# Performance work log

Measured on AMD Instinct MI355X. Metric: run time of the kernel, lower is better.

Reference implementation:

```python
import jax, jax.numpy as jnp
import numpy as np

B, S, D, H = 2, 2048, 1024, 16
DK = D // H
ROPE_BASE = 10000.0


def _rope_cos_sin(seq_len, dim, dtype):
    inv_freq = 1.0 / (ROPE_BASE ** (jnp.arange(0, dim, 2, dtype=jnp.float32) / dim))
    t = jnp.arange(seq_len, dtype=jnp.float32)
    freqs = jnp.outer(t, inv_freq)              # [S, dim/2]
    emb = jnp.concatenate([freqs, freqs], -1)   # [S, dim]
    return jnp.cos(emb).astype(dtype), jnp.sin(emb).astype(dtype)


def _rotate_half(x):
    x1, x2 = jnp.split(x, 2, axis=-1)
    return jnp.concatenate([-x2, x1], axis=-1)


def setup_inputs() -> dict:
    key = jax.random.key(0)
    ks = jax.random.split(key, 7)
    q = jax.random.normal(ks[0], (B, S, D), jnp.float32)
    k = jax.random.normal(ks[1], (B, S, D), jnp.float32)
    v = jax.random.normal(ks[2], (B, S, D), jnp.float32)
    scale = 0.02
    Wq = jax.random.normal(ks[3], (D, D), jnp.float32) * scale
    Wk = jax.random.normal(ks[4], (D, D), jnp.float32) * scale
    Wv = jax.random.normal(ks[5], (D, D), jnp.float32) * scale
    Wo = jax.random.normal(ks[6], (D, D), jnp.float32) * scale
    mask = jnp.tril(jnp.ones((S, S), jnp.int32))[None, None]  # [1,1,S,S] causal 0/1
    return {"q": q, "k": k, "v": v, "Wq": Wq, "Wk": Wk, "Wv": Wv, "Wo": Wo, "mask": mask}


def reference(q, k, v, Wq, Wk, Wv, Wo, mask):
    def proj(x, W):
        # nn.Linear: x @ W.T ; then [B,S,H,DK] -> [B,H,S,DK]
        return (x @ W.T).reshape(B, S, H, DK).transpose(0, 2, 1, 3)

    qh, kh, vh = proj(q, Wq), proj(k, Wk), proj(v, Wv)

    cos, sin = _rope_cos_sin(S, DK, qh.dtype)   # [S, DK]
    qh = qh * cos + _rotate_half(qh) * sin
    kh = kh * cos + _rotate_half(kh) * sin

    scores = jnp.einsum("bhqd,bhkd->bhqk", qh, kh) / jnp.sqrt(jnp.asarray(DK, qh.dtype))
    scores = jnp.where(mask == 0, jnp.asarray(-1000.0, scores.dtype), scores)
    attn = jax.nn.softmax(scores, axis=-1)      # dropout=0 (eval)
    out = jnp.einsum("bhqk,bhkd->bhqd", attn, vh)
    out = out.transpose(0, 2, 1, 3).reshape(B, S, D)
    return out @ Wo.T
```

## Files before the change

### kernel.cpp

```cpp
#include <hip/hip_runtime.h>
#include <hip/hip_bf16.h>
#include <stdint.h>

#define Bdim 2
#define Sdim 2048
#define Ddim 1024
#define Hdim 16

typedef unsigned short u16;
typedef __bf16 bf16x8 __attribute__((ext_vector_type(8)));
typedef float f32x4 __attribute__((ext_vector_type(4)));

__device__ __forceinline__ u16 f2b(float x) {
  return __builtin_bit_cast(u16, (__bf16)x);
}
__device__ __forceinline__ float b2f(u16 u) {
  return __bfloat162float(__builtin_bit_cast(__hip_bfloat16, u));
}
__device__ __forceinline__ f32x4 mfma_bf16(bf16x8 a, bf16x8 b, f32x4 c) {
  return __builtin_amdgcn_mfma_f32_16x16x32_bf16(a, b, c, 0, 0, 0);
}
__device__ __forceinline__ void gload_lds16(const u16* gp, u16* lp) {
  __builtin_amdgcn_global_load_lds(
      (const __attribute__((address_space(1))) void*)gp,
      (__attribute__((address_space(3))) void*)lp, 16, 0, 0);
}

__global__ __launch_bounds__(256) void k_convert(
    const float* __restrict__ q, const float* __restrict__ k, const float* __restrict__ v,
    const float* __restrict__ wq, const float* __restrict__ wk,
    const float* __restrict__ wv, const float* __restrict__ wo,
    u16* __restrict__ qb, u16* __restrict__ kb, u16* __restrict__ vb,
    u16* __restrict__ wqb, u16* __restrict__ wkb, u16* __restrict__ wvb, u16* __restrict__ wob) {
  int i = (blockIdx.x * 256 + threadIdx.x) * 4;
  const float* src;
  u16* dst;
  int off;
  if (i < 12582912) {
    int s = i >> 22;
    off = i - (s << 22);
    src = (s == 0) ? q : ((s == 1) ? k : v);
    dst = (s == 0) ? qb : ((s == 1) ? kb : vb);
  } else {
    int j = i - 12582912;
    int s = j >> 20;
    off = j - (s << 20);
    src = (s == 0) ? wq : ((s == 1) ? wk : ((s == 2) ? wv : wo));
    dst = (s == 0) ? wqb : ((s == 1) ? wkb : ((s == 2) ? wvb : wob));
  }
  float4 f = *(const float4*)(src + off);
  ushort4 o;
  o.x = f2b(f.x); o.y = f2b(f.y); o.z = f2b(f.z); o.w = f2b(f.w);
  *(ushort4*)(dst + off) = o;
}

__global__ __launch_bounds__(256) void k_ropetab(float* __restrict__ cosT, float* __restrict__ sinT) {
  int i = blockIdx.x * 256 + threadIdx.x;
  int s = i >> 5, j = i & 31;
  float invf = expf(-(float)j * 0.28782313662425574f);
  float ang = (float)s * invf;
  float sn, cs;
  sincosf(ang, &sn, &cs);
  cosT[i] = cs;
  sinT[i] = sn;
}

template <int OUTF>
__global__ __launch_bounds__(256) void k_gemm(
    const u16* __restrict__ A0, const u16* __restrict__ W0, void* __restrict__ O0,
    const u16* __restrict__ A1, const u16* __restrict__ W1, void* __restrict__ O1,
    const u16* __restrict__ A2, const u16* __restrict__ W2, void* __restrict__ O2) {
  const u16* A = (blockIdx.z == 0) ? A0 : ((blockIdx.z == 1) ? A1 : A2);
  const u16* W = (blockIdx.z == 0) ? W0 : ((blockIdx.z == 1) ? W1 : W2);
  void* O = (blockIdx.z == 0) ? O0 : ((blockIdx.z == 1) ? O1 : O2);

  __shared__ u16 As[128 * 32];
  __shared__ u16 Bs[128 * 32];

  const int tid = threadIdx.x;
  const int wave = tid >> 6, lane = tid & 63;
  const int g = lane >> 4, cc = lane & 15;
  const int wm = wave >> 1, wn = wave & 1;
  const int row0 = blockIdx.x * 128, col0 = blockIdx.y * 128;

  const int srow = wave * 16 + (lane >> 2);
  const int sseg = (lane & 3) * 8;
  const u16* Ap  = A + (size_t)(row0 + srow) * 1024 + sseg;
  const u16* Ap2 = Ap + 64 * 1024;
  const u16* Wp  = W + (size_t)(col0 + srow) * 1024 + sseg;
  const u16* Wp2 = Wp + 64 * 1024;
  u16* asl  = &As[wave * 512];
  u16* asl2 = &As[2048 + wave * 512];
  u16* bsl  = &Bs[wave * 512];
  u16* bsl2 = &Bs[2048 + wave * 512];

  f32x4 acc[4][4] = {};

  for (int k0 = 0; k0 < 1024; k0 += 32) {
    __syncthreads();
    gload_lds16(Ap + k0, asl);
    gload_lds16(Ap2 + k0, asl2);
    gload_lds16(Wp + k0, bsl);
    gload_lds16(Wp2 + k0, bsl2);
    __syncthreads();
    bf16x8 af[4], bfv[4];
#pragma unroll
    for (int mi = 0; mi < 4; ++mi)
      af[mi] = *(const bf16x8*)&As[(wm * 64 + mi * 16 + cc) * 32 + g * 8];
#pragma unroll
    for (int ni = 0; ni < 4; ++ni)
      bfv[ni] = *(const bf16x8*)&Bs[(wn * 64 + ni * 16 + cc) * 32 + g * 8];
#pragma unroll
    for (int mi = 0; mi < 4; ++mi)
#pragma unroll
      for (int ni = 0; ni < 4; ++ni)
        acc[mi][ni] = mfma_bf16(af[mi], bfv[ni], acc[mi][ni]);
  }

#pragma unroll
  for (int mi = 0; mi < 4; ++mi)
#pragma unroll
    for (int ni = 0; ni < 4; ++ni)
#pragma unroll
      for (int r = 0; r < 4; ++r) {
        const int row = row0 + wm * 64 + mi * 16 + g * 4 + r;
        const int col = col0 + wn * 64 + ni * 16 + cc;
        const float vv = acc[mi][ni][r];
        if (OUTF)
          ((float*)O)[row * 1024 + col] = vv;
        else
          ((u16*)O)[row * 1024 + col] = f2b(vv);
      }
}

__global__ __launch_bounds__(256) void k_rope(
    const u16* __restrict__ tq, const u16* __restrict__ tk,
    const float* __restrict__ cosT, const float* __restrict__ sinT,
    u16* __restrict__ Qr, u16* __restrict__ Kr) {
  int idx = blockIdx.x * 256 + threadIdx.x;
  int t = idx >> 21;
  int r = idx & ((1 << 21) - 1);
  int j = r & 31;
  int h = (r >> 5) & 15;
  int s = (r >> 9) & 2047;
  int b = (r >> 20) & 1;

  const u16* in = t ? tk : tq;
  u16* out = t ? Kr : Qr;

  int bi = (b * Sdim + s) * Ddim + h * 64 + j;
  float x1 = b2f(in[bi]);
  float x2 = b2f(in[bi + 32]);
  float cv = cosT[s * 32 + j];
  float sv = sinT[s * 32 + j];
  float o1 = x1 * cv - x2 * sv;
  float o2 = x2 * cv + x1 * sv;
  if (t == 0) { o1 *= 0.18033688011112042f; o2 *= 0.18033688011112042f; }
  int bo = ((b * Hdim + h) * Sdim + s) * 64 + j;
  out[bo] = f2b(o1);
  out[bo + 32] = f2b(o2);
}

__global__ __launch_bounds__(256) void k_transv(const u16* __restrict__ tv, u16* __restrict__ Vt) {
  __shared__ u16 tl[64][72];
  const int bh = blockIdx.y;
  const int b = bh >> 4, h = bh & 15;
  const int s0 = blockIdx.x * 64;
  const int tid = threadIdx.x;
#pragma unroll
  for (int p = 0; p < 4; ++p) {
    int row = p * 16 + (tid >> 4);
    int dc = (tid & 15) * 4;
    ushort4 val = *(const ushort4*)(tv + (b * Sdim + s0 + row) * Ddim + h * 64 + dc);
    *(ushort4*)&tl[row][dc] = val;
  }
  __syncthreads();
#pragma unroll
  for (int p = 0; p < 4; ++p) {
    int dr = p * 16 + (tid >> 4);
    int sc = (tid & 15) * 4;
    ushort4 o;
    o.x = tl[sc + 0][dr];
    o.y = tl[sc + 1][dr];
    o.z = tl[sc + 2][dr];
    o.w = tl[sc + 3][dr];
    int s_abs = s0 + sc;
    int cch = s_abs >> 5;
    int kap = s_abs & 31;
    int g2 = (kap >> 2) & 3;
    int seg = kap >> 4;
    *(ushort4*)(Vt + (size_t)(bh * 64 + dr) * Sdim + (cch << 5) + (g2 << 3) + (seg << 2)) = o;
  }
}

template <int M0, int M1>
__device__ __forceinline__ void attn_chunk64(
    const u16* __restrict__ kl, const u16* __restrict__ vl, int cc, int g,
    const bf16x8 qf[4],
    float& mold0, float& mold1, float& lsum0, float& lsum1,
    f32x4 ot0[4], f32x4 ot1[4]) {
  const int m7 = cc & 7;
  const int gA = (g ^ m7) * 8;
  const int gB = ((g + 4) ^ m7) * 8;

  f32x4 x0A0 = {}, x0B0 = {}, x0A1 = {}, x0B1 = {};
  {
    const u16* r0 = kl + cc * 64;
    const u16* r1 = kl + (16 + cc) * 64;
    bf16x8 k0 = *(const bf16x8*)(r0 + gA);
    bf16x8 k1 = *(const bf16x8*)(r0 + gB);
    bf16x8 k2 = *(const bf16x8*)(r1 + gA);
    bf16x8 k3 = *(const bf16x8*)(r1 + gB);
    x0A0 = mfma_bf16(k0, qf[0], x0A0);
    x0A0 = mfma_bf16(k1, qf[1], x0A0);
    x0B0 = mfma_bf16(k2, qf[0], x0B0);
    x0B0 = mfma_bf16(k3, qf[1], x0B0);
    x0A1 = mfma_bf16(k0, qf[2], x0A1);
    x0A1 = mfma_bf16(k1, qf[3], x0A1);
    x0B1 = mfma_bf16(k2, qf[2], x0B1);
    x0B1 = mfma_bf16(k3, qf[3], x0B1);
  }
  f32x4 x1A0 = {}, x1B0 = {}, x1A1 = {}, x1B1 = {};
  if (M1 != 2) {
    const u16* r0 = kl + (32 + cc) * 64;
    const u16* r1 = kl + (48 + cc) * 64;
    bf16x8 k0 = *(const bf16x8*)(r0 + gA);
    bf16x8 k1 = *(const bf16x8*)(r0 + gB);
    bf16x8 k2 = *(const bf16x8*)(r1 + gA);
    bf16x8 k3 = *(const bf16x8*)(r1 + gB);
    x1A0 = mfma_bf16(k0, qf[0], x1A0);
    x1A0 = mfma_bf16(k1, qf[1], x1A0);
    x1B0 = mfma_bf16(k2, qf[0], x1B0);
    x1B0 = mfma_bf16(k3, qf[1], x1B0);
    x1A1 = mfma_bf16(k0, qf[2], x1A1);
    x1A1 = mfma_bf16(k1, qf[3], x1A1);
    x1B1 = mfma_bf16(k2, qf[2], x1B1);
    x1B1 = mfma_bf16(k3, qf[3], x1B1);
  }

  float p0[16], p1[16];
#pragma unroll
  for (int r = 0; r < 4; ++r) {
    const int ka = g * 4 + r;
    float a0 = x0A0[r], b0 = x0B0[r], a1 = x0A1[r], b1 = x0B1[r];
    if (M0 == 1) {
      a0 = (ka <= cc) ? a0 : -30000.0f;
      b0 = -30000.0f;
      b1 = (ka <= cc) ? b1 : -30000.0f;
    }
    p0[r] = a0; p0[4 + r] = b0;
    p1[r] = a1; p1[4 + r] = b1;
  }
  if (M1 != 2) {
#pragma unroll
    for (int r = 0; r < 4; ++r) {
      const int ka = g * 4 + r;
      float a0 = x1A0[r], b0 = x1B0[r], a1 = x1A1[r], b1 = x1B1[r];
      if (M1 == 1) {
        a0 = (ka <= cc) ? a0 : -30000.0f;
        b0 = -30000.0f;
        b1 = (ka <= cc) ? b1 : -30000.0f;
      }
      p0[8 + r] = a0; p0[12 + r] = b0;
      p1[8 + r] = a1; p1[12 + r] = b1;
    }
  }
  const int NP = (M1 == 2) ? 8 : 16;
  float m0 = p0[0], m1 = p1[0];
#pragma unroll
  for (int j = 1; j < 16; ++j)
    if (j < NP) { m0 = fmaxf(m0, p0[j]); m1 = fmaxf(m1, p1[j]); }

  if (!__all((m0 <= mold0 + 11.5f) && (m1 <= mold1 + 11.5f))) {
    float M0v = fmaxf(m0, __shfl_xor(m0, 16));
    M0v = fmaxf(M0v, __shfl_xor(M0v, 32));
    float M1v = fmaxf(m1, __shfl_xor(m1, 16));
    M1v = fmaxf(M1v, __shfl_xor(M1v, 32));
    M0v = fmaxf(mold0, M0v);
    M1v = fmaxf(mold1, M1v);
    const float al0 = exp2f(mold0 - M0v), al1 = exp2f(mold1 - M1v);
    mold0 = M0v; mold1 = M1v;
    lsum0 *= al0; lsum1 *= al1;
#pragma unroll
    for (int dc = 0; dc < 4; ++dc) { ot0[dc] *= al0; ot1[dc] *= al1; }
  }

  float rs0 = 0.f, rs1 = 0.f;
  bf16x8 a0v, a1v, b0v2, b1v2;
#pragma unroll
  for (int j = 0; j < 8; ++j) {
    float e0 = exp2f(p0[j] - mold0);
    float e1 = exp2f(p1[j] - mold1);
    rs0 += e0; rs1 += e1;
    a0v[j] = (__bf16)e0;
    a1v[j] = (__bf16)e1;
  }
  if (M1 != 2) {
#pragma unroll
    for (int j = 0; j < 8; ++j) {
      float e0 = exp2f(p0[8 + j] - mold0);
      float e1 = exp2f(p1[8 + j] - mold1);
      rs0 += e0; rs1 += e1;
      b0v2[j] = (__bf16)e0;
      b1v2[j] = (__bf16)e1;
    }
  }
  lsum0 += rs0; lsum1 += rs1;

#pragma unroll
  for (int dc = 0; dc < 4; ++dc) {
    bf16x8 vv = *(const bf16x8*)(vl + (dc * 16 + cc) * 64 + gA);
    ot0[dc] = mfma_bf16(vv, a0v, ot0[dc]);
    ot1[dc] = mfma_bf16(vv, a1v, ot1[dc]);
  }
  if (M1 != 2) {
#pragma unroll
    for (int dc = 0; dc < 4; ++dc) {
      bf16x8 vv = *(const bf16x8*)(vl + (dc * 16 + cc) * 64 + gB);
      ot0[dc] = mfma_bf16(vv, b0v2, ot0[dc]);
      ot1[dc] = mfma_bf16(vv, b1v2, ot1[dc]);
    }
  }
}

__global__ __launch_bounds__(256, 2) void k_attn(
    const u16* __restrict__ Qr, const u16* __restrict__ Kr,
    const u16* __restrict__ Vt, u16* __restrict__ Oc,
    float* __restrict__ PO, float* __restrict__ PML) {
  __shared__ u16 Kl[2][4096];
  __shared__ u16 Vl[2][4096];

  const int x = blockIdx.x;
  const int bh = x & 31;
  const int slot = x >> 5;
  const int p = slot & 7;
  const int half = slot >> 3;
  const int iH = 15 - p, iL = p;
  const int nH = 2 * iH + 2;
  const int b = bh >> 4, h = bh & 15;
  const int tid = threadIdx.x;
  const int w = tid >> 6;
  const int lane = tid & 63;
  const int g = lane >> 4, cc = lane & 15;

  const u16* Kp = Kr + (size_t)bh * (Sdim * 64);
  const u16* Vp = Vt + (size_t)bh * (64 * Sdim);

  const int rloc = lane >> 3;
  const int sg = (lane & 7) ^ rloc;
  const u16* kS = Kp + (size_t)(w * 16 + rloc) * 64 + sg * 8;
  const u16* vS = Vp + (size_t)(w * 16 + rloc) * 2048 + sg * 8;

  auto stageKV = [&](int t, int buf) {
    const size_t ko = (size_t)t * 4096;
    const size_t vo = (size_t)t * 64;
    gload_lds16(kS + ko, &Kl[buf][w * 1024]);
    gload_lds16(kS + ko + 512, &Kl[buf][w * 1024 + 512]);
    gload_lds16(vS + vo, &Vl[buf][w * 1024]);
    gload_lds16(vS + vo + 16384, &Vl[buf][w * 1024 + 512]);
  };

  auto runseg = [&](int tile, int c0, int c1, int part) {
    const int myDiag = 2 * tile + (w >> 1);
    const u16* Qp = Qr + (size_t)(bh * Sdim + tile * 128 + w * 32) * 64;
    bf16x8 qf[4];
    qf[0] = *(const bf16x8*)(Qp + cc * 64 + g * 8);
    qf[1] = *(const bf16x8*)(Qp + cc * 64 + g * 8 + 32);
    qf[2] = *(const bf16x8*)(Qp + (16 + cc) * 64 + g * 8);
    qf[3] = *(const bf16x8*)(Qp + (16 + cc) * 64 + g * 8 + 32);

    float mold0 = -1e30f, mold1 = -1e30f, lsum0 = 0.f, lsum1 = 0.f;
    f32x4 ot0[4] = {}, ot1[4] = {};

    __syncthreads();
    stageKV(c0, c0 & 1);
    for (int t = c0; t < c1; ++t) {
      __syncthreads();
      if (t + 1 < c1) stageKV(t + 1, (t + 1) & 1);
      if (t <= myDiag) {
        const u16* kl = &Kl[t & 1][0];
        const u16* vl = &Vl[t & 1][0];
        if (t < myDiag)
          attn_chunk64<0, 0>(kl, vl, cc, g, qf, mold0, mold1, lsum0, lsum1, ot0, ot1);
        else if (w & 1)
          attn_chunk64<0, 1>(kl, vl, cc, g, qf, mold0, mold1, lsum0, lsum1, ot0, ot1);
        else
          attn_chunk64<1, 2>(kl, vl, cc, g, qf, mold0, mold1, lsum0, lsum1, ot0, ot1);
      }
    }

    float l0 = lsum0 + __shfl_xor(lsum0, 16);
    l0 += __shfl_xor(l0, 32);
    float l1 = lsum1 + __shfl_xor(lsum1, 16);
    l1 += __shfl_xor(l1, 32);

    if (part < 0) {
      const float rl0 = 1.0f / l0, rl1 = 1.0f / l1;
      u16* dst0 = Oc + (size_t)(b * Sdim + tile * 128 + w * 32 + cc) * Ddim + h * 64 + g * 4;
      u16* dst1 = dst0 + 16 * Ddim;
#pragma unroll
      for (int dc = 0; dc < 4; ++dc) {
        ushort4 o0, o1;
        o0.x = f2b(ot0[dc][0] * rl0);
        o0.y = f2b(ot0[dc][1] * rl0);
        o0.z = f2b(ot0[dc][2] * rl0);
        o0.w = f2b(ot0[dc][3] * rl0);
        o1.x = f2b(ot1[dc][0] * rl1);
        o1.y = f2b(ot1[dc][1] * rl1);
        o1.z = f2b(ot1[dc][2] * rl1);
        o1.w = f2b(ot1[dc][3] * rl1);
        *(ushort4*)(dst0 + dc * 16) = o0;
        *(ushort4*)(dst1 + dc * 16) = o1;
      }
    } else {
      const int slotp = (bh * 7 + p) * 2 + part;
      float* po0 = PO + (size_t)slotp * 8192 + (w * 32 + cc) * 64;
      float* po1 = po0 + 16 * 64;
#pragma unroll
      for (int dc = 0; dc < 4; ++dc) {
        *(f32x4*)(po0 + dc * 16 + g * 4) = ot0[dc];
        *(f32x4*)(po1 + dc * 16 + g * 4) = ot1[dc];
      }
      if (g == 0) {
        float* ml = PML + (size_t)slotp * 256 + (w * 32 + cc) * 2;
        ml[0] = mold0;
        ml[1] = l0;
        ml[32] = mold1;
        ml[33] = l1;
      }
    }
  };

  if (half == 0) {
    runseg(iH, 0, (nH < 18) ? nH : 18, (nH > 18) ? 0 : -1);
  } else {
    if (p < 7) runseg(iH, 18, nH, 1);
    runseg(iL, 0, 2 * iL + 2, -1);
  }
}

__global__ __launch_bounds__(128) void k_comb(
    const float* __restrict__ PO, const float* __restrict__ PML,
    u16* __restrict__ Oc) {
  const int x = blockIdx.x;
  const int bh = x / 7, p = x % 7;
  const int b = bh >> 4, h = bh & 15;
  const int iH = 15 - p;
  const int row = threadIdx.x;
  const float* ml0 = PML + (size_t)(x * 2 + 0) * 256 + row * 2;
  const float* ml1 = PML + (size_t)(x * 2 + 1) * 256 + row * 2;
  const float m0 = ml0[0], l0 = ml0[1];
  const float m1 = ml1[0], l1 = ml1[1];
  const float M = fmaxf(m0, m1);
  float e0 = exp2f(m0 - M), e1 = exp2f(m1 - M);
  const float inv = 1.0f / (e0 * l0 + e1 * l1);
  e0 *= inv; e1 *= inv;
  const float* O0 = PO + (size_t)(x * 2 + 0) * 8192 + row * 64;
  const float* O1 = PO + (size_t)(x * 2 + 1) * 8192 + row * 64;
  u16* dst = Oc + (size_t)(b * Sdim + iH * 128 + row) * Ddim + h * 64;
#pragma unroll
  for (int c = 0; c < 64; c += 4) {
    float4 a = *(const float4*)(O0 + c);
    float4 bb = *(const float4*)(O1 + c);
    ushort4 o;
    o.x = f2b(a.x * e0 + bb.x * e1);
    o.y = f2b(a.y * e0 + bb.y * e1);
    o.z = f2b(a.z * e0 + bb.z * e1);
    o.w = f2b(a.w * e0 + bb.w * e1);
    *(ushort4*)(dst + c) = o;
  }
}

extern "C" void kernel_launch(void* const* d_in, const int* in_sizes, int n_in,
                              void* d_out, int out_size, void* d_ws, size_t ws_size,
                              hipStream_t stream) {
  const float* q = (const float*)d_in[0];
  const float* k = (const float*)d_in[1];
  const float* v = (const float*)d_in[2];
  const float* wq = (const float*)d_in[3];
  const float* wk = (const float*)d_in[4];
  const float* wv = (const float*)d_in[5];
  const float* wo = (const float*)d_in[6];
  float* out = (float*)d_out;

  uint8_t* ws = (uint8_t*)d_ws;
  const size_t MiB = 1ull << 20;
  u16* qb  = (u16*)(ws + 0 * MiB);
  u16* kb  = (u16*)(ws + 8 * MiB);
  u16* vb  = (u16*)(ws + 16 * MiB);
  u16* wqb = (u16*)(ws + 24 * MiB);
  u16* wkb = (u16*)(ws + 26 * MiB);
  u16* wvb = (u16*)(ws + 28 * MiB);
  u16* wob = (u16*)(ws + 30 * MiB);
  u16* tQ  = (u16*)(ws + 32 * MiB);
  u16* tK  = (u16*)(ws + 40 * MiB);
  u16* tV  = (u16*)(ws + 48 * MiB);
  u16* Qr  = (u16*)(ws + 56 * MiB);
  u16* Kr  = (u16*)(ws + 64 * MiB);
  u16* Vt  = (u16*)(ws + 72 * MiB);
  u16* Oc  = (u16*)(ws + 80 * MiB);
  float* cosT = (float*)(ws + 88 * MiB);
  float* sinT = (float*)(ws + 88 * MiB + 256 * 1024);
  float* PO  = (float*)(ws + 0 * MiB);
  float* PML = (float*)(ws + 15 * MiB);

  k_convert<<<16384, 256, 0, stream>>>(q, k, v, wq, wk, wv, wo,
                                       qb, kb, vb, wqb, wkb, wvb, wob);
  k_ropetab<<<256, 256, 0, stream>>>(cosT, sinT);
  k_gemm<0><<<dim3(32, 8, 3), 256, 0, stream>>>(qb, wqb, tQ, kb, wkb, tK, vb, wvb, tV);
  k_rope<<<16384, 256, 0, stream>>>(tQ, tK, cosT, sinT, Qr, Kr);
  k_transv<<<dim3(32, 32), 256, 0, stream>>>(tV, Vt);
  k_attn<<<512, 256, 0, stream>>>(Qr, Kr, Vt, Oc, PO, PML);
  k_comb<<<224, 128, 0, stream>>>(PO, PML, Oc);
  k_gemm<1><<<dim3(32, 8, 1), 256, 0, stream>>>(Oc, wob, out, Oc, wob, out, Oc, wob, out);
}
```

Before: 134.7 us.

## Split causal attention into finer balanced KV segments and swizzle GEMM blocks

Attention work is re-partitioned with constant tables into 40 segments per head (1280 blocks), with longer query tiles split into up to four KV ranges. Partial outputs are stored in bf16 and merged by a generalized combine kernel. The aim is better load balance and occupancy across CUs; occupancy is also raised via launch_bounds 4. GEMM blocks are remapped with an XCD-aware swizzle of a 1D grid to improve L2 locality. The costs are extra partial-output traffic, a combine pass that reads up to four partials, and some precision loss from storing partials in bf16.

```diff
diff --git a/kernel.cpp b/kernel.cpp
--- a/kernel.cpp
+++ b/kernel.cpp
@@ -25,6 +25,17 @@
       (const __attribute__((address_space(1))) void*)gp,
       (__attribute__((address_space(3))) void*)lp, 16, 0, 0);
 }
+
+__constant__ uint8_t PT_tile[40] = {
+  0,1,2,3, 4,4, 5,5, 6,6, 7,7, 8,8,8, 9,9,9, 10,10,10, 11,11,11,
+  12,12,12,12, 13,13,13,13, 14,14,14,14, 15,15,15,15};
+__constant__ uint8_t PT_c0[40] = {
+  0,0,0,0, 0,5, 0,6, 0,7, 0,8, 0,6,12, 0,7,14, 0,8,15, 0,8,16,
+  0,7,14,20, 0,7,14,21, 0,8,16,23, 0,8,16,24};
+__constant__ uint8_t PT_c1[40] = {
+  2,4,6,8, 5,10, 6,12, 7,14, 8,16, 6,12,18, 7,14,20, 8,15,22, 8,16,24,
+  7,14,20,26, 7,14,21,28, 8,16,23,30, 8,16,24,32};
+__constant__ uint8_t CB_base[12] = {0,2,4,6,8,11,14,17,20,24,28,32};
 
 __global__ __launch_bounds__(256) void k_convert(
     const float* __restrict__ q, const float* __restrict__ k, const float* __restrict__ v,
@@ -70,9 +81,17 @@
     const u16* __restrict__ A0, const u16* __restrict__ W0, void* __restrict__ O0,
     const u16* __restrict__ A1, const u16* __restrict__ W1, void* __restrict__ O1,
     const u16* __restrict__ A2, const u16* __restrict__ W2, void* __restrict__ O2) {
-  const u16* A = (blockIdx.z == 0) ? A0 : ((blockIdx.z == 1) ? A1 : A2);
-  const u16* W = (blockIdx.z == 0) ? W0 : ((blockIdx.z == 1) ? W1 : W2);
-  void* O = (blockIdx.z == 0) ? O0 : ((blockIdx.z == 1) ? O1 : O2);
+  const int id = blockIdx.x;
+  const int cpx = gridDim.x >> 3;
+  const int swz = (id & 7) * cpx + (id >> 3);
+  const int z = swz >> 8;
+  const int rem = swz & 255;
+  const int row0 = (rem & 31) * 128;
+  const int col0 = (rem >> 5) * 128;
+
+  const u16* A = (z == 0) ? A0 : ((z == 1) ? A1 : A2);
+  const u16* W = (z == 0) ? W0 : ((z == 1) ? W1 : W2);
+  void* O = (z == 0) ? O0 : ((z == 1) ? O1 : O2);
 
   __shared__ u16 As[128 * 32];
   __shared__ u16 Bs[128 * 32];
@@ -81,7 +100,6 @@
   const int wave = tid >> 6, lane = tid & 63;
   const int g = lane >> 4, cc = lane & 15;
   const int wm = wave >> 1, wn = wave & 1;
-  const int row0 = blockIdx.x * 128, col0 = blockIdx.y * 128;
 
   const int srow = wave * 16 + (lane >> 2);
   const int sseg = (lane & 3) * 8;
@@ -323,28 +341,32 @@
   }
 }
 
-__global__ __launch_bounds__(256, 2) void k_attn(
+__global__ __launch_bounds__(256, 4) void k_attn(
     const u16* __restrict__ Qr, const u16* __restrict__ Kr,
     const u16* __restrict__ Vt, u16* __restrict__ Oc,
-    float* __restrict__ PO, float* __restrict__ PML) {
+    u16* __restrict__ PO, float* __restrict__ PML) {
   __shared__ u16 Kl[2][4096];
   __shared__ u16 Vl[2][4096];
 
   const int x = blockIdx.x;
   const int bh = x & 31;
-  const int slot = x >> 5;
-  const int p = slot & 7;
-  const int half = slot >> 3;
-  const int iH = 15 - p, iL = p;
-  const int nH = 2 * iH + 2;
+  const int u = 39 - (x >> 5);
+  const int tile = PT_tile[u];
+  const int c0 = PT_c0[u];
+  const int c1 = PT_c1[u];
+  const int slot = u - 4;
   const int b = bh >> 4, h = bh & 15;
   const int tid = threadIdx.x;
   const int w = tid >> 6;
   const int lane = tid & 63;
   const int g = lane >> 4, cc = lane & 15;
 
+  const int qrow0 = tile * 128 + w * 32;
+  const int myDiag = 2 * tile + (w >> 1);
+
   const u16* Kp = Kr + (size_t)bh * (Sdim * 64);
   const u16* Vp = Vt + (size_t)bh * (64 * Sdim);
+  const u16* Qp = Qr + (size_t)(bh * Sdim + qrow0) * 64;
 
   const int rloc = lane >> 3;
   const int sg = (lane & 7) ^ rloc;
@@ -360,113 +382,127 @@
     gload_lds16(vS + vo + 16384, &Vl[buf][w * 1024 + 512]);
   };
 
-  auto runseg = [&](int tile, int c0, int c1, int part) {
-    const int myDiag = 2 * tile + (w >> 1);
-    const u16* Qp = Qr + (size_t)(bh * Sdim + tile * 128 + w * 32) * 64;
-    bf16x8 qf[4];
-    qf[0] = *(const bf16x8*)(Qp + cc * 64 + g * 8);
-    qf[1] = *(const bf16x8*)(Qp + cc * 64 + g * 8 + 32);
-    qf[2] = *(const bf16x8*)(Qp + (16 + cc) * 64 + g * 8);
-    qf[3] = *(const bf16x8*)(Qp + (16 + cc) * 64 + g * 8 + 32);
-
-    float mold0 = -1e30f, mold1 = -1e30f, lsum0 = 0.f, lsum1 = 0.f;
-    f32x4 ot0[4] = {}, ot1[4] = {};
-
+  bf16x8 qf[4];
+  qf[0] = *(const bf16x8*)(Qp + cc * 64 + g * 8);
+  qf[1] = *(const bf16x8*)(Qp + cc * 64 + g * 8 + 32);
+  qf[2] = *(const bf16x8*)(Qp + (16 + cc) * 64 + g * 8);
+  qf[3] = *(const bf16x8*)(Qp + (16 + cc) * 64 + g * 8 + 32);
+
+  float mold0 = -1e30f, mold1 = -1e30f, lsum0 = 0.f, lsum1 = 0.f;
+  f32x4 ot0[4] = {}, ot1[4] = {};
+
+  stageKV(c0, c0 & 1);
+  for (int t = c0; t < c1; ++t) {
     __syncthreads();
-    stageKV(c0, c0 & 1);
-    for (int t = c0; t < c1; ++t) {
-      __syncthreads();
-      if (t + 1 < c1) stageKV(t + 1, (t + 1) & 1);
-      if (t <= myDiag) {
-        const u16* kl = &Kl[t & 1][0];
-        const u16* vl = &Vl[t & 1][0];
-        if (t < myDiag)
-          attn_chunk64<0, 0>(kl, vl, cc, g, qf, mold0, mold1, lsum0, lsum1, ot0, ot1);
-        else if (w & 1)
-          attn_chunk64<0, 1>(kl, vl, cc, g, qf, mold0, mold1, lsum0, lsum1, ot0, ot1);
-        else
-          attn_chunk64<1, 2>(kl, vl, cc, g, qf, mold0, mold1, lsum0, lsum1, ot0, ot1);
-      }
-    }
-
-    float l0 = lsum0 + __shfl_xor(lsum0, 16);
-    l0 += __shfl_xor(l0, 32);
-    float l1 = lsum1 + __shfl_xor(lsum1, 16);
-    l1 += __shfl_xor(l1, 32);
-
-    if (part < 0) {
-      const float rl0 = 1.0f / l0, rl1 = 1.0f / l1;
-      u16* dst0 = Oc + (size_t)(b * Sdim + tile * 128 + w * 32 + cc) * Ddim + h * 64 + g * 4;
-      u16* dst1 = dst0 + 16 * Ddim;
-#pragma unroll
-      for (int dc = 0; dc < 4; ++dc) {
-        ushort4 o0, o1;
-        o0.x = f2b(ot0[dc][0] * rl0);
-        o0.y = f2b(ot0[dc][1] * rl0);
-        o0.z = f2b(ot0[dc][2] * rl0);
-        o0.w = f2b(ot0[dc][3] * rl0);
-        o1.x = f2b(ot1[dc][0] * rl1);
-        o1.y = f2b(ot1[dc][1] * rl1);
-        o1.z = f2b(ot1[dc][2] * rl1);
-        o1.w = f2b(ot1[dc][3] * rl1);
-        *(ushort4*)(dst0 + dc * 16) = o0;
-        *(ushort4*)(dst1 + dc * 16) = o1;
-      }
-    } else {
-      const int slotp = (bh * 7 + p) * 2 + part;
-      float* po0 = PO + (size_t)slotp * 8192 + (w * 32 + cc) * 64;
-      float* po1 = po0 + 16 * 64;
-#pragma unroll
-      for (int dc = 0; dc < 4; ++dc) {
-        *(f32x4*)(po0 + dc * 16 + g * 4) = ot0[dc];
-        *(f32x4*)(po1 + dc * 16 + g * 4) = ot1[dc];
-      }
-      if (g == 0) {
-        float* ml = PML + (size_t)slotp * 256 + (w * 32 + cc) * 2;
-        ml[0] = mold0;
-        ml[1] = l0;
-        ml[32] = mold1;
-        ml[33] = l1;
-      }
-    }
-  };
-
-  if (half == 0) {
-    runseg(iH, 0, (nH < 18) ? nH : 18, (nH > 18) ? 0 : -1);
+    if (t + 1 < c1) stageKV(t + 1, (t + 1) & 1);
+    if (t <= myDiag) {
+      const u16* kl = &Kl[t & 1][0];
+      const u16* vl = &Vl[t & 1][0];
+      if (t < myDiag)
+        attn_chunk64<0, 0>(kl, vl, cc, g, qf, mold0, mold1, lsum0, lsum1, ot0, ot1);
+      else if (w & 1)
+        attn_chunk64<0, 1>(kl, vl, cc, g, qf, mold0, mold1, lsum0, lsum1, ot0, ot1);
+      else
+        attn_chunk64<1, 2>(kl, vl, cc, g, qf, mold0, mold1, lsum0, lsum1, ot0, ot1);
+    }
+  }
+
+  float l0 = lsum0 + __shfl_xor(lsum0, 16);
+  l0 += __shfl_xor(l0, 32);
+  float l1 = lsum1 + __shfl_xor(lsum1, 16);
+  l1 += __shfl_xor(l1, 32);
+
+  if (slot < 0) {
+    const float rl0 = 1.0f / l0, rl1 = 1.0f / l1;
+    u16* dst0 = Oc + (size_t)(b * Sdim + qrow0 + cc) * Ddim + h * 64 + g * 4;
+    u16* dst1 = dst0 + 16 * Ddim;
+#pragma unroll
+    for (int dc = 0; dc < 4; ++dc) {
+      ushort4 o0, o1;
+      o0.x = f2b(ot0[dc][0] * rl0);
+      o0.y = f2b(ot0[dc][1] * rl0);
+      o0.z = f2b(ot0[dc][2] * rl0);
+      o0.w = f2b(ot0[dc][3] * rl0);
+      o1.x = f2b(ot1[dc][0] * rl1);
+      o1.y = f2b(ot1[dc][1] * rl1);
+      o1.z = f2b(ot1[dc][2] * rl1);
+      o1.w = f2b(ot1[dc][3] * rl1);
+      *(ushort4*)(dst0 + dc * 16) = o0;
+      *(ushort4*)(dst1 + dc * 16) = o1;
+    }
   } else {
-    if (p < 7) runseg(iH, 18, nH, 1);
-    runseg(iL, 0, 2 * iL + 2, -1);
+    const int sgl = bh * 36 + slot;
+    u16* po0 = PO + (size_t)sgl * 8192 + (w * 32 + cc) * 64;
+    u16* po1 = po0 + 16 * 64;
+#pragma unroll
+    for (int dc = 0; dc < 4; ++dc) {
+      ushort4 o0, o1;
+      o0.x = f2b(ot0[dc][0]); o0.y = f2b(ot0[dc][1]);
+      o0.z = f2b(ot0[dc][2]); o0.w = f2b(ot0[dc][3]);
+      o1.x = f2b(ot1[dc][0]); o1.y = f2b(ot1[dc][1]);
+      o1.z = f2b(ot1[dc][2]); o1.w = f2b(ot1[dc][3]);
+      *(ushort4*)(po0 + dc * 16 + g * 4) = o0;
+      *(ushort4*)(po1 + dc * 16 + g * 4) = o1;
+    }
+    if (g == 0) {
+      float* ml = PML + (size_t)sgl * 256 + (w * 32 + cc) * 2;
+      ml[0] = mold0;
+      ml[1] = l0;
+      ml[32] = mold1;
+      ml[33] = l1;
+    }
   }
 }
 
 __global__ __launch_bounds__(128) void k_comb(
-    const float* __restrict__ PO, const float* __restrict__ PML,
+    const u16* __restrict__ PO, const float* __restrict__ PML,
     u16* __restrict__ Oc) {
   const int x = blockIdx.x;
-  const int bh = x / 7, p = x % 7;
+  const int bh = x & 31;
+  const int tidx = x >> 5;
+  const int tile = tidx + 4;
+  const int cnt = (tidx >> 2) + 2;
+  const int sgb = bh * 36 + CB_base[tidx];
   const int b = bh >> 4, h = bh & 15;
-  const int iH = 15 - p;
-  const int row = threadIdx.x;
-  const float* ml0 = PML + (size_t)(x * 2 + 0) * 256 + row * 2;
-  const float* ml1 = PML + (size_t)(x * 2 + 1) * 256 + row * 2;
-  const float m0 = ml0[0], l0 = ml0[1];
-  const float m1 = ml1[0], l1 = ml1[1];
-  const float M = fmaxf(m0, m1);
-  float e0 = exp2f(m0 - M), e1 = exp2f(m1 - M);
-  const float inv = 1.0f / (e0 * l0 + e1 * l1);
-  e0 *= inv; e1 *= inv;
-  const float* O0 = PO + (size_t)(x * 2 + 0) * 8192 + row * 64;
-  const float* O1 = PO + (size_t)(x * 2 + 1) * 8192 + row * 64;
-  u16* dst = Oc + (size_t)(b * Sdim + iH * 128 + row) * Ddim + h * 64;
+  const int r = threadIdx.x;
+
+  float m[4], l[4];
+#pragma unroll
+  for (int j = 0; j < 4; ++j) {
+    if (j < cnt) {
+      const float* ml = PML + (size_t)(sgb + j) * 256 + r * 2;
+      m[j] = ml[0];
+      l[j] = ml[1];
+    } else { m[j] = -1e30f; l[j] = 0.f; }
+  }
+  float M = fmaxf(fmaxf(m[0], m[1]), fmaxf(m[2], m[3]));
+  float wgt[4];
+  float ltot = 0.f;
+#pragma unroll
+  for (int j = 0; j < 4; ++j) {
+    wgt[j] = (j < cnt) ? exp2f(m[j] - M) : 0.f;
+    ltot += wgt[j] * l[j];
+  }
+  const float inv = 1.0f / ltot;
+#pragma unroll
+  for (int j = 0; j < 4; ++j) wgt[j] *= inv;
+
+  u16* dst = Oc + (size_t)(b * Sdim + tile * 128 + r) * Ddim + h * 64;
 #pragma unroll
   for (int c = 0; c < 64; c += 4) {
-    float4 a = *(const float4*)(O0 + c);
-    float4 bb = *(const float4*)(O1 + c);
+    float acc0 = 0.f, acc1 = 0.f, acc2 = 0.f, acc3 = 0.f;
+#pragma unroll
+    for (int j = 0; j < 4; ++j) {
+      if (j < cnt) {
+        ushort4 pv = *(const ushort4*)(PO + (size_t)(sgb + j) * 8192 + r * 64 + c);
+        acc0 += wgt[j] * b2f(pv.x);
+        acc1 += wgt[j] * b2f(pv.y);
+        acc2 += wgt[j] * b2f(pv.z);
+        acc3 += wgt[j] * b2f(pv.w);
+      }
+    }
     ushort4 o;
-    o.x = f2b(a.x * e0 + bb.x * e1);
-    o.y = f2b(a.y * e0 + bb.y * e1);
-    o.z = f2b(a.z * e0 + bb.z * e1);
-    o.w = f2b(a.w * e0 + bb.w * e1);
+    o.x = f2b(acc0); o.y = f2b(acc1); o.z = f2b(acc2); o.w = f2b(acc3);
     *(ushort4*)(dst + c) = o;
   }
 }
@@ -501,16 +537,16 @@
   u16* Oc  = (u16*)(ws + 80 * MiB);
   float* cosT = (float*)(ws + 88 * MiB);
   float* sinT = (float*)(ws + 88 * MiB + 256 * 1024);
-  float* PO  = (float*)(ws + 0 * MiB);
-  float* PML = (float*)(ws + 15 * MiB);
+  u16*   PO  = (u16*)(ws + 32 * MiB);
+  float* PML = (float*)(ws + 51 * MiB);
 
   k_convert<<<16384, 256, 0, stream>>>(q, k, v, wq, wk, wv, wo,
                                        qb, kb, vb, wqb, wkb, wvb, wob);
   k_ropetab<<<256, 256, 0, stream>>>(cosT, sinT);
-  k_gemm<0><<<dim3(32, 8, 3), 256, 0, stream>>>(qb, wqb, tQ, kb, wkb, tK, vb, wvb, tV);
+  k_gemm<0><<<768, 256, 0, stream>>>(qb, wqb, tQ, kb, wkb, tK, vb, wvb, tV);
   k_rope<<<16384, 256, 0, stream>>>(tQ, tK, cosT, sinT, Qr, Kr);
   k_transv<<<dim3(32, 32), 256, 0, stream>>>(tV, Vt);
-  k_attn<<<512, 256, 0, stream>>>(Qr, Kr, Vt, Oc, PO, PML);
-  k_comb<<<224, 128, 0, stream>>>(PO, PML, Oc);
-  k_gemm<1><<<dim3(32, 8, 1), 256, 0, stream>>>(Oc, wob, out, Oc, wob, out, Oc, wob, out);
-}
+  k_attn<<<1280, 256, 0, stream>>>(Qr, Kr, Vt, Oc, PO, PML);
+  k_comb<<<384, 128, 0, stream>>>(PO, PML, Oc);
+  k_gemm<1><<<256, 256, 0, stream>>>(Oc, wob, out, Oc, wob, out, Oc, wob, out);
+}
```

Result: slower. 160.2 us (+18.9%).
